# Kernel optimization log

Hardware: AMD Instinct MI355X
Metric: run time of the kernel (lower is better)

## Reference

```python
import jax, jax.numpy as jnp
import numpy as np

B, N, E = 8, 1000, 16000
HIST, PRED = 8, 12
IN_DIM = 14          # pm25(1) + met features(13)
HID_GAT, HEADS = 256, 8
GNN_OUT = 13
HID = 64             # GRU hidden (self.hid_dim = 64 in source)


def setup_inputs() -> dict:
    key = jax.random.key(0)
    ks = jax.random.split(key, 20)
    p = lambda k, shp, s=0.05: jax.random.normal(k, shp, dtype=jnp.float32) * s
    return {
        "pm25_hist": jax.random.normal(ks[0], (B, HIST, N, 1), dtype=jnp.float32),
        "feature": jax.random.normal(ks[1], (B, HIST + PRED, N, IN_DIM - 1), dtype=jnp.float32),
        "edge_index": jax.random.randint(ks[2], (2, E), 0, N),
        "gat1_W": p(ks[3], (IN_DIM, HEADS * HID_GAT)),
        "gat1_att_src": p(ks[4], (HEADS, HID_GAT)),
        "gat1_att_dst": p(ks[5], (HEADS, HID_GAT)),
        "gat1_b": p(ks[6], (HEADS * HID_GAT,)),
        "gat2_W": p(ks[7], (HEADS * HID_GAT, GNN_OUT)),
        "gat2_att_src": p(ks[8], (1, GNN_OUT)),
        "gat2_att_dst": p(ks[9], (1, GNN_OUT)),
        "gat2_b": p(ks[10], (GNN_OUT,)),
        "gru_W_ih": p(ks[11], (3 * HID, IN_DIM + GNN_OUT)),
        "gru_W_hh": p(ks[12], (3 * HID, HID)),
        "gru_b_ih": p(ks[13], (3 * HID,)),
        "gru_b_hh": p(ks[14], (3 * HID,)),
        "fc_out_W": p(ks[15], (HID, 1)),
        "fc_out_b": p(ks[16], (1,)),
    }


def _gat_conv(x, W, a_src, a_dst, b, src, dst, concat):
    # Single-graph GATConv (PyG semantics, eval mode: dropout disabled).
    # x: [N, F_in]; src/dst: [E'] (self-loops already appended)
    H, D = a_src.shape
    h = (x @ W).reshape(N, H, D)                       # [N, H, D]
    e = jax.nn.leaky_relu(
        (h * a_src).sum(-1)[src] + (h * a_dst).sum(-1)[dst], 0.2
    )                                                  # [E', H]
    # segment softmax over incoming edges of each dst node
    m = jax.ops.segment_max(e, dst, num_segments=N)
    ex = jnp.exp(e - m[dst])
    alpha = ex / jax.ops.segment_sum(ex, dst, num_segments=N)[dst]
    out = jax.ops.segment_sum(alpha[:, :, None] * h[src], dst, num_segments=N)  # [N, H, D]
    return (out.reshape(N, H * D) + b) if concat else (out.mean(1) + b)


def reference(pm25_hist, feature, edge_index,
              gat1_W, gat1_att_src, gat1_att_dst, gat1_b,
              gat2_W, gat2_att_src, gat2_att_dst, gat2_b,
              gru_W_ih, gru_W_hh, gru_b_ih, gru_b_hh,
              fc_out_W, fc_out_b):
    # add self-loops (PyG GATConv default)
    loop = jnp.arange(N)
    src = jnp.concatenate([edge_index[0], loop])
    dst = jnp.concatenate([edge_index[1], loop])

    def gnn(x):  # x: [N, IN_DIM] -> [N, GNN_OUT]
        h = jax.nn.elu(_gat_conv(x, gat1_W, gat1_att_src, gat1_att_dst, gat1_b, src, dst, True))
        return _gat_conv(h, gat2_W, gat2_att_src, gat2_att_dst, gat2_b, src, dst, False)

    gnn_b = jax.vmap(gnn)

    def gru(x, h):  # torch.nn.GRUCell math
        i_r, i_z, i_n = jnp.split(x @ gru_W_ih.T + gru_b_ih, 3, axis=-1)
        h_r, h_z, h_n = jnp.split(h @ gru_W_hh.T + gru_b_hh, 3, axis=-1)
        r = jax.nn.sigmoid(i_r + h_r)
        z = jax.nn.sigmoid(i_z + h_z)
        n = jnp.tanh(i_n + r * h_n)
        return (1.0 - z) * n + z * h

    feats = jnp.moveaxis(feature[:, HIST:HIST + PRED], 1, 0)  # [PRED, B, N, 13]

    def step(carry, f_t):
        hn, xn = carry
        x = jnp.concatenate([xn, f_t], axis=-1)               # [B, N, IN_DIM]
        g = gnn_b(x)                                          # [B, N, GNN_OUT]
        gx = jnp.concatenate([g, x], axis=-1).reshape(B * N, IN_DIM + GNN_OUT)
        hn = gru(gx, hn)                                      # [B*N, HID]
        xn = hn.reshape(B, N, HID) @ fc_out_W + fc_out_b      # [B, N, 1]
        return (hn, xn), xn

    h0 = jnp.zeros((B * N, HID), jnp.float32)
    xn0 = pm25_hist[:, -1]                                    # [B, N, 1]
    _, preds = jax.lax.scan(step, (h0, xn0), feats)
    return jnp.moveaxis(preds, 0, 1)                          # [B, PRED, N, 1]
```

## Files before the change

### kernel.cpp

```cpp
#include <hip/hip_runtime.h>
#include <hip/hip_bf16.h>
#include <math.h>

#define BB 8
#define NN 1000
#define EE 16000
#define ETOT 17000
#define TPRED 12
#define FEAT 13
#define INDIM 14
#define HEADS 8
#define HG 256
#define C1 2048
#define GO 13
#define HID 64

typedef unsigned int  uint32;
typedef unsigned short ushort16;
typedef uint32 uvec4 __attribute__((ext_vector_type(4)));
typedef __fp16 hf2 __attribute__((ext_vector_type(2)));

union U32H2 { uint32 u; hf2 h; };
__device__ __forceinline__ hf2 u2h(uint32 u){ U32H2 c; c.u=u; return c.h; }
__device__ __forceinline__ uint32 h2u(hf2 h){ U32H2 c; c.h=h; return c.u; }

#if __has_builtin(__builtin_amdgcn_fdot2)
__device__ __forceinline__ float FDOT2(hf2 a, hf2 b, float c){
    return __builtin_amdgcn_fdot2(a, b, c, false);
}
#else
__device__ __forceinline__ float FDOT2(hf2 a, hf2 b, float c){
    return c + (float)a.x*(float)b.x + (float)a.y*(float)b.y;
}
#endif

__device__ __forceinline__ float lrelu(float v){ return v > 0.f ? v : 0.2f*v; }

__device__ __forceinline__ ushort16 f2bf(float f){
    union { float f; uint32 u; } v; v.f = f;
    uint32 r = v.u + 0x7FFFu + ((v.u >> 16) & 1u);
    return (ushort16)(r >> 16);
}
__device__ __forceinline__ uint32 pack2(float lo, float hi){
    return (uint32)f2bf(lo) | ((uint32)f2bf(hi) << 16);
}
__device__ __forceinline__ void cvt2(uint32 u, float& lo, float& hi){
    union { uint32 u; float f; } a, b;
    a.u = u << 16; b.u = u & 0xFFFF0000u;
    lo = a.f; hi = b.f;
}


__global__ void k_att1pre(const float* W1, const float* asrc, const float* adst,
                          float* Wsrc, float* Wdst){
    int k = blockIdx.x >> 3, h = blockIdx.x & 7;
    int tid = threadIdx.x;
    float wv = W1[k*C1 + h*HG + tid];
    float ps = wv * asrc[h*HG + tid];
    float pd = wv * adst[h*HG + tid];
    #pragma unroll
    for (int m=1;m<64;m<<=1){ ps += __shfl_xor(ps,m); pd += __shfl_xor(pd,m); }
    __shared__ float rs[4], rd[4];
    int w = tid>>6;
    if ((tid&63)==0){ rs[w]=ps; rd[w]=pd; }
    __syncthreads();
    if (tid==0){
        Wsrc[k*8+h] = rs[0]+rs[1]+rs[2]+rs[3];
        Wdst[k*8+h] = rd[0]+rd[1]+rd[2]+rd[3];
    }
}

__global__ void k_packW1(const float* W1, uint32* w1pk){
    int i = blockIdx.x*blockDim.x + threadIdx.x;
    if (i < C1*8){
        int c = i >> 3, kk = i & 7;
        float lo = (kk < 7) ? W1[(2*kk)*C1 + c]   : 0.f;
        float hi = (kk < 7) ? W1[(2*kk+1)*C1 + c] : 0.f;
        w1pk[i] = h2u(__builtin_amdgcn_cvt_pkrtz(lo, hi));
    }
}

__global__ void k_att2pre(const float* W2, const float* a2s, const float* a2d,
                          uint32* w2pk){
    int m = blockIdx.x*blockDim.x + threadIdx.x;
    if (m < C1/2){
        int c0 = 2*m, c1 = 2*m+1;
        float colA[16], colB[16];
        float ssA=0.f, ddA=0.f, ssB=0.f, ddB=0.f;
        #pragma unroll
        for (int j=0;j<GO;j++){
            float wA = W2[c0*GO+j], wB = W2[c1*GO+j];
            colA[j]=wA; colB[j]=wB;
            ssA += wA*a2s[j]; ddA += wA*a2d[j];
            ssB += wB*a2s[j]; ddB += wB*a2d[j];
        }
        colA[13]=ssA; colA[14]=ddA; colA[15]=0.f;
        colB[13]=ssB; colB[14]=ddB; colB[15]=0.f;
        #pragma unroll
        for (int j=0;j<16;j++)
            w2pk[m*16+j] = h2u(__builtin_amdgcn_cvt_pkrtz(colA[j], colB[j]));
    }
}

__global__ void k_init(const float* pm25, const float* feat,
                       const float* Wsrc, const float* Wdst,
                       float* hn, float* xn, int* count,
                       float* ssrc, float* sdst, uint32* xpk){
    int i = blockIdx.x*blockDim.x + threadIdx.x;
    if (i < BB*NN*HID) hn[i] = 0.f;
    if (i < NN) count[i] = 0;
    if (i < BB*NN){
        int b = i/NN, n = i%NN;
        float x[INDIM];
        x[0] = pm25[(b*8 + 7)*NN + n];
        xn[i] = x[0];
        const float* fp = feat + ((size_t)(b*20 + 8)*NN + n)*FEAT;
        #pragma unroll
        for (int k=0;k<FEAT;k++) x[k+1] = fp[k];
        #pragma unroll
        for (int h=0;h<8;h++){
            float ss=0.f, dd=0.f;
            #pragma unroll
            for (int k=0;k<INDIM;k++){ ss += x[k]*Wsrc[k*8+h]; dd += x[k]*Wdst[k*8+h]; }
            ssrc[i*8+h] = ss; sdst[i*8+h] = dd;
        }
        #pragma unroll
        for (int p=0;p<7;p++) xpk[i*8+p] = pack2(x[2*p], x[2*p+1]);
        xpk[i*8+7] = 0u;
    }
}

__global__ void k_count(const int* ei, int* count){
    int e = blockIdx.x*blockDim.x + threadIdx.x;
    if (e < ETOT){
        int dst = (e<EE) ? ei[EE+e] : (e-EE);
        atomicAdd(&count[dst], 1);
    }
}

__global__ void k_scan(const int* count, int* offs, int* cursor){
    __shared__ int s[1024];
    int tid = threadIdx.x;
    int myc = (tid<NN) ? count[tid] : 0;
    s[tid] = myc;
    __syncthreads();
    for (int d=1; d<1024; d<<=1){
        int v = (tid>=d) ? s[tid-d] : 0;
        __syncthreads();
        s[tid] += v;
        __syncthreads();
    }
    if (tid<NN){
        int off = s[tid] - myc;
        offs[tid] = off; cursor[tid] = off;
    }
    if (tid==NN-1) offs[NN] = s[tid];
}

__global__ void k_fill(const int* ei, int* cursor, int* csr_src){
    int e = blockIdx.x*blockDim.x + threadIdx.x;
    if (e < ETOT){
        int src = (e<EE) ? ei[e]    : (e-EE);
        int dst = (e<EE) ? ei[EE+e] : (e-EE);
        int pos = atomicAdd(&cursor[dst], 1);
        csr_src[pos] = src;
    }
}


__global__ __launch_bounds__(64) void k_agg14(const uint32* xpk, const float* ssrc,
        const float* sdst, const int* offs, const int* csr, float* agg){
    int lane = threadIdx.x;
    int blk = blockIdx.x;
    int b = blk & 7, dstn = blk >> 3;
    int bn = b*NN + dstn;
    int base = offs[dstn], deg = offs[dstn+1]-base;
    int h = lane & 7, slot = lane >> 3;
    float sdd = sdst[bn*8 + h];
    float mloc = -1e30f;
    for (int i=slot;i<deg;i+=8){
        int s = csr[base+i];
        mloc = fmaxf(mloc, lrelu(ssrc[(b*NN+s)*8+h]+sdd));
    }
    mloc = fmaxf(mloc, __shfl_xor(mloc,8));
    mloc = fmaxf(mloc, __shfl_xor(mloc,16));
    mloc = fmaxf(mloc, __shfl_xor(mloc,32));
    float dloc = 0.f;
    for (int i=slot;i<deg;i+=8){
        int s = csr[base+i];
        dloc += __expf(lrelu(ssrc[(b*NN+s)*8+h]+sdd)-mloc);
    }
    dloc += __shfl_xor(dloc,8); dloc += __shfl_xor(dloc,16); dloc += __shfl_xor(dloc,32);
    float rden = 1.f/dloc;
    int kk = lane & 7, h2 = lane >> 3;
    float m2   = __shfl(mloc, h2);
    float r2   = __shfl(rden, h2);
    float sdd2 = __shfl(sdd,  h2);
    float a0=0.f, a1=0.f;
    for (int e=0;e<deg;e++){
        int s = csr[base+e];
        float sc = lrelu(ssrc[(b*NN+s)*8+h2] + sdd2);
        float al = __expf(sc - m2)*r2;
        float x0,x1; cvt2(xpk[(b*NN+s)*8+kk], x0, x1);
        a0 += al*x0; a1 += al*x1;
    }
    float2 st; st.x = a0; st.y = a1;
    *(float2*)(agg + (size_t)bn*128 + h2*16 + 2*kk) = st;
}

__global__ __launch_bounds__(256,1) void k_expand(const float* agg, const uint32* w1pk,
        const uint32* w2pk, const float* b1, float* h2o, float* s2s, float* s2d){
    int tid = threadIdx.x;
    int hh = tid >> 5;
    uint32 w1r[64];
    #pragma unroll
    for (int q=0;q<16;q++){
        uvec4 u = *(const uvec4*)(w1pk + tid*64 + 4*q);
        w1r[4*q]=u.x; w1r[4*q+1]=u.y; w1r[4*q+2]=u.z; w1r[4*q+3]=u.w;
    }
    uint32 w2r[64];
    #pragma unroll
    for (int q=0;q<16;q++){
        uvec4 u = *(const uvec4*)(w2pk + tid*64 + 4*q);
        w2r[4*q]=u.x; w2r[4*q+1]=u.y; w2r[4*q+2]=u.z; w2r[4*q+3]=u.w;
    }
    float b1r[8];
    #pragma unroll
    for (int j=0;j<8;j++) b1r[j] = b1[8*tid+j];
    __shared__ float sred[256*17];
    __shared__ float red2[64];
    for (int idx = blockIdx.x; idx < BB*NN; idx += gridDim.x){
        const float4* ap = (const float4*)(agg + (size_t)idx*128 + hh*16);
        float4 A0=ap[0], A1=ap[1], A2=ap[2], A3=ap[3];
        hf2 agh[7];
        agh[0]=__builtin_amdgcn_cvt_pkrtz(A0.x,A0.y);
        agh[1]=__builtin_amdgcn_cvt_pkrtz(A0.z,A0.w);
        agh[2]=__builtin_amdgcn_cvt_pkrtz(A1.x,A1.y);
        agh[3]=__builtin_amdgcn_cvt_pkrtz(A1.z,A1.w);
        agh[4]=__builtin_amdgcn_cvt_pkrtz(A2.x,A2.y);
        agh[5]=__builtin_amdgcn_cvt_pkrtz(A2.z,A2.w);
        agh[6]=__builtin_amdgcn_cvt_pkrtz(A3.x,A3.y);
        float v[8];
        #pragma unroll
        for (int j=0;j<8;j++){
            float s = b1r[j];
            #pragma unroll
            for (int kk=0;kk<7;kk++) s = FDOT2(agh[kk], u2h(w1r[j*8+kk]), s);
            v[j] = s > 0.f ? s : __expf(s) - 1.f;
        }
        hf2 vp[4];
        #pragma unroll
        for (int q=0;q<4;q++) vp[q] = __builtin_amdgcn_cvt_pkrtz(v[2*q], v[2*q+1]);
        #pragma unroll
        for (int j=0;j<16;j++){
            float s = 0.f;
            #pragma unroll
            for (int q=0;q<4;q++) s = FDOT2(vp[q], u2h(w2r[q*16+j]), s);
            sred[tid*17 + j] = s;
        }
        __syncthreads();
        int j = tid & 15, g = tid >> 4;
        float s = 0.f;
        #pragma unroll
        for (int i=0;i<16;i++) s += sred[(g + 16*i)*17 + j];
        s += __shfl_xor(s, 16);
        s += __shfl_xor(s, 32);
        int lane = tid & 63, w = tid >> 6;
        if (lane < 16) red2[w*16 + lane] = s;
        __syncthreads();
        if (tid < 15){
            float r = red2[tid] + red2[16+tid] + red2[32+tid] + red2[48+tid];
            if (tid < GO)      h2o[idx*GO + tid] = r;
            else if (tid==13)  s2s[idx] = r;
            else               s2d[idx] = r;
        }
        __syncthreads();
    }
}

__global__ __launch_bounds__(256) void k_tail(int t, int last,
        const float* feat, const int* offs, const int* csr,
        const float* h2, const float* s2src, const float* s2dst, const float* b2,
        const float* Wih, const float* Whh, const float* bih, const float* bhh,
        const float* fcw, const float* fcb, const float* Wsrc, const float* Wdst,
        float* hn, float* xn, float* out,
        float* ssrc, float* sdst, uint32* xpk){
    __shared__ float sWih[192*27];
    __shared__ float sWhh[192*65];
    __shared__ float sb[449];
    __shared__ float sWa[224];
    __shared__ float gxs[4][28];
    __shared__ float hs[4][64];
    int tid = threadIdx.x;
    for (int i=tid;i<192*27;i+=256) sWih[i] = Wih[i];
    for (int i=tid;i<192*64;i+=256) sWhh[(i>>6)*65 + (i&63)] = Whh[i];
    for (int i=tid;i<192;i+=256){ sb[i] = bih[i]; sb[192+i] = bhh[i]; }
    if (tid<64) sb[384+tid] = fcw[tid];
    if (tid==0) sb[448] = fcb[0];
    if (tid<112){ sWa[tid] = Wsrc[tid]; sWa[112+tid] = Wdst[tid]; }
    __syncthreads();
    int w = tid>>6, lane = tid&63;
    for (int i=0;i<4;i++){
        int bn = blockIdx.x*16 + i*4 + w;
        int b = bn/NN, n = bn%NN;
        int base = offs[n], deg = offs[n+1]-base;
        float sdd = s2dst[bn];
        float mloc = -1e30f;
        for (int e=lane;e<deg;e+=64){
            int s = csr[base+e];
            mloc = fmaxf(mloc, lrelu(s2src[b*NN+s] + sdd));
        }
        #pragma unroll
        for (int m=1;m<64;m<<=1) mloc = fmaxf(mloc, __shfl_xor(mloc,m));
        float dloc = 0.f;
        for (int e=lane;e<deg;e+=64){
            int s = csr[base+e];
            dloc += __expf(lrelu(s2src[b*NN+s] + sdd) - mloc);
        }
        #pragma unroll
        for (int m=1;m<64;m<<=1) dloc += __shfl_xor(dloc,m);
        float rdv = 1.f / dloc;
        float acc[GO];
        #pragma unroll
        for (int c=0;c<GO;c++) acc[c]=0.f;
        for (int e=lane;e<deg;e+=64){
            int s = csr[base+e];
            float al = __expf(lrelu(s2src[b*NN+s] + sdd) - mloc) * rdv;
            const float* hr = h2 + (size_t)(b*NN+s)*GO;
            #pragma unroll
            for (int c=0;c<GO;c++) acc[c] += al*hr[c];
        }
        #pragma unroll
        for (int c=0;c<GO;c++){
            #pragma unroll
            for (int m=1;m<64;m<<=1) acc[c] += __shfl_xor(acc[c],m);
        }
        if (lane==0){
            #pragma unroll
            for (int c=0;c<GO;c++) gxs[w][c] = acc[c] + b2[c];
            gxs[w][GO] = xn[bn];
        }
        if (lane>=14 && lane<27)
            gxs[w][lane] = feat[((size_t)(b*20 + 8 + t)*NN + n)*FEAT + (lane-14)];
        hs[w][lane] = hn[bn*HID + lane];
        __syncthreads();
        float ir = sb[lane], iz = sb[64+lane], inn = sb[128+lane];
        #pragma unroll
        for (int c=0;c<27;c++){
            float xv = gxs[w][c];
            ir  += sWih[lane*27        + c]*xv;
            iz  += sWih[(64+lane)*27   + c]*xv;
            inn += sWih[(128+lane)*27  + c]*xv;
        }
        float hr = sb[192+lane], hz = sb[256+lane], hnv = sb[320+lane];
        #pragma unroll
        for (int j=0;j<64;j++){
            float hv = hs[w][j];
            hr  += sWhh[lane*65        + j]*hv;
            hz  += sWhh[(64+lane)*65   + j]*hv;
            hnv += sWhh[(128+lane)*65  + j]*hv;
        }
        float r  = 1.f/(1.f+__expf(-(ir+hr)));
        float z  = 1.f/(1.f+__expf(-(iz+hz)));
        float nv = tanhf(inn + r*hnv);
        float hold = hs[w][lane];
        float hnew = (1.f - z)*nv + z*hold;
        hn[bn*HID+lane] = hnew;
        float xv = hnew * sb[384+lane];
        #pragma unroll
        for (int m=1;m<64;m<<=1) xv += __shfl_xor(xv,m);
        float res = xv + sb[448];
        if (lane==0){
            xn[bn] = res;
            out[(b*TPRED + t)*NN + n] = res;
        }
        if (!last){
            const float* fp = feat + ((size_t)(b*20 + 9 + t)*NN + n)*FEAT;
            if (lane < 16){
                int h = lane & 7;
                const float* Wa = (lane<8) ? sWa : sWa+112;
                float s = res * Wa[h];
                #pragma unroll
                for (int k=1;k<14;k++) s += fp[k-1]*Wa[k*8+h];
                if (lane<8) ssrc[bn*8+h] = s; else sdst[bn*8+h] = s;
            } else if (lane < 23){
                int p = lane - 16;
                float lo = (p==0) ? res : fp[2*p-1];
                float hi = fp[2*p];
                xpk[bn*8+p] = pack2(lo, hi);
            } else if (lane == 23){
                xpk[bn*8+7] = 0u;
            }
        }
        __syncthreads();
    }
}


extern "C" void kernel_launch(void* const* d_in, const int* in_sizes, int n_in,
                              void* d_out, int out_size, void* d_ws, size_t ws_size,
                              hipStream_t stream){
    const float* pm25 = (const float*)d_in[0];
    const float* feat = (const float*)d_in[1];
    const int*   ei   = (const int*)  d_in[2];
    const float* W1   = (const float*)d_in[3];
    const float* a1s  = (const float*)d_in[4];
    const float* a1d  = (const float*)d_in[5];
    const float* b1   = (const float*)d_in[6];
    const float* W2   = (const float*)d_in[7];
    const float* a2s  = (const float*)d_in[8];
    const float* a2d  = (const float*)d_in[9];
    const float* b2   = (const float*)d_in[10];
    const float* Wih  = (const float*)d_in[11];
    const float* Whh  = (const float*)d_in[12];
    const float* bih  = (const float*)d_in[13];
    const float* bhh  = (const float*)d_in[14];
    const float* fcw  = (const float*)d_in[15];
    const float* fcb  = (const float*)d_in[16];
    float* out = (float*)d_out;

    float* f = (float*)d_ws;
    size_t o = 0;
    float* ssrc1 = f+o; o += (size_t)BB*NN*8;
    float* sdst1 = f+o; o += (size_t)BB*NN*8;
    float* agg   = f+o; o += (size_t)BB*NN*128;
    float* h2    = f+o; o += (size_t)BB*NN*GO + 8;
    float* s2s   = f+o; o += (size_t)BB*NN;
    float* s2d   = f+o; o += (size_t)BB*NN;
    float* hn    = f+o; o += (size_t)BB*NN*HID;
    float* xn    = f+o; o += (size_t)BB*NN;
    float* Wsrc  = f+o; o += INDIM*8;
    float* Wdst  = f+o; o += INDIM*8;
    uint32* xpk  = (uint32*)(f+o); o += (size_t)BB*NN*8;
    uint32* w1pk = (uint32*)(f+o); o += (size_t)C1*8;
    uint32* w2pk = (uint32*)(f+o); o += (size_t)(C1/2)*16;
    int* ibase  = (int*)(f+o);
    int* count  = ibase;
    int* cursor = ibase + NN;
    int* offs   = ibase + 2*NN;
    int* csr    = ibase + 2*NN + NN + 1;

    k_att1pre<<<112, 256,0,stream>>>(W1, a1s, a1d, Wsrc, Wdst);
    k_packW1 <<<64,  256,0,stream>>>(W1, w1pk);
    k_att2pre<<<4,   256,0,stream>>>(W2, a2s, a2d, w2pk);
    k_init   <<<2000,256,0,stream>>>(pm25, feat, Wsrc, Wdst, hn, xn, count,
                                     ssrc1, sdst1, xpk);
    k_count  <<<67,  256,0,stream>>>(ei, count);
    k_scan   <<<1,  1024,0,stream>>>(count, offs, cursor);
    k_fill   <<<67,  256,0,stream>>>(ei, cursor, csr);

    for (int t=0; t<TPRED; t++){
        k_agg14  <<<8000, 64,0,stream>>>(xpk, ssrc1, sdst1, offs, csr, agg);
        k_expand <<<512, 256,0,stream>>>(agg, w1pk, w2pk, b1, h2, s2s, s2d);
        k_tail   <<<500, 256,0,stream>>>(t, (t==TPRED-1)?1:0, feat, offs, csr,
                                         h2, s2s, s2d, b2,
                                         Wih, Whh, bih, bhh, fcw, fcb, Wsrc, Wdst,
                                         hn, xn, out, ssrc1, sdst1, xpk);
    }
}
```

Baseline: 940.5 us.

## Use packed fp16 dot products and smaller LDS footprint in GRU tail kernel

The GRU tail kernel now stores W_ih, W_hh, the input vector and hidden state as packed fp16 pairs in shared memory and accumulates with fp16 dot2 instructions. This halves the per-block LDS footprint and the LDS reads in the matvec. Occupancy is raised via launch_bounds(256,4), and the grid doubles to 1000 blocks with 8 nodes each instead of 16. The cost is reduced GRU matvec precision and weight staging into LDS repeated across twice as many blocks.

```diff
diff --git a/kernel.cpp b/kernel.cpp
--- a/kernel.cpp
+++ b/kernel.cpp
@@ -48,6 +48,9 @@
     union { uint32 u; float f; } a, b;
     a.u = u << 16; b.u = u & 0xFFFF0000u;
     lo = a.f; hi = b.f;
+}
+__device__ __forceinline__ uint32 pkh(float lo, float hi){
+    hf2 h; h.x = (__fp16)lo; h.y = (__fp16)hi; return h2u(h);
 }
 
 
@@ -278,30 +281,39 @@
     }
 }
 
-__global__ __launch_bounds__(256) void k_tail(int t, int last,
+__global__ __launch_bounds__(256,4) void k_tail(int t, int last,
         const float* feat, const int* offs, const int* csr,
         const float* h2, const float* s2src, const float* s2dst, const float* b2,
         const float* Wih, const float* Whh, const float* bih, const float* bhh,
         const float* fcw, const float* fcb, const float* Wsrc, const float* Wdst,
         float* hn, float* xn, float* out,
         float* ssrc, float* sdst, uint32* xpk){
-    __shared__ float sWih[192*27];
-    __shared__ float sWhh[192*65];
-    __shared__ float sb[449];
-    __shared__ float sWa[224];
-    __shared__ float gxs[4][28];
-    __shared__ float hs[4][64];
+    __shared__ uint32 sWihP[192*14];
+    __shared__ uint32 sWhhP[192*33];
+    __shared__ float  sb[449];
+    __shared__ float  sWa[224];
+    __shared__ float  gxs[4][28];
+    __shared__ uint32 gxsP[4][14];
+    __shared__ uint32 hsP[4][32];
     int tid = threadIdx.x;
-    for (int i=tid;i<192*27;i+=256) sWih[i] = Wih[i];
-    for (int i=tid;i<192*64;i+=256) sWhh[(i>>6)*65 + (i&63)] = Whh[i];
+    for (int i=tid;i<192*14;i+=256){
+        int r = i/14, c2 = i - r*14;
+        float lo = Wih[r*27 + 2*c2];
+        float hi = (2*c2+1 < 27) ? Wih[r*27 + 2*c2 + 1] : 0.f;
+        sWihP[i] = pkh(lo, hi);
+    }
+    for (int i=tid;i<192*32;i+=256){
+        int r = i>>5, j2 = i&31;
+        sWhhP[r*33 + j2] = pkh(Whh[r*64 + 2*j2], Whh[r*64 + 2*j2 + 1]);
+    }
     for (int i=tid;i<192;i+=256){ sb[i] = bih[i]; sb[192+i] = bhh[i]; }
     if (tid<64) sb[384+tid] = fcw[tid];
     if (tid==0) sb[448] = fcb[0];
     if (tid<112){ sWa[tid] = Wsrc[tid]; sWa[112+tid] = Wdst[tid]; }
     __syncthreads();
     int w = tid>>6, lane = tid&63;
-    for (int i=0;i<4;i++){
-        int bn = blockIdx.x*16 + i*4 + w;
+    for (int i=0;i<2;i++){
+        int bn = blockIdx.x*8 + i*4 + w;
         int b = bn/NN, n = bn%NN;
         int base = offs[n], deg = offs[n+1]-base;
         float sdd = s2dst[bn];
@@ -326,9 +338,9 @@
         for (int e=lane;e<deg;e+=64){
             int s = csr[base+e];
             float al = __expf(lrelu(s2src[b*NN+s] + sdd) - mloc) * rdv;
-            const float* hr = h2 + (size_t)(b*NN+s)*GO;
-            #pragma unroll
-            for (int c=0;c<GO;c++) acc[c] += al*hr[c];
+            const float* hr2 = h2 + (size_t)(b*NN+s)*GO;
+            #pragma unroll
+            for (int c=0;c<GO;c++) acc[c] += al*hr2[c];
         }
         #pragma unroll
         for (int c=0;c<GO;c++){
@@ -339,31 +351,35 @@
             #pragma unroll
             for (int c=0;c<GO;c++) gxs[w][c] = acc[c] + b2[c];
             gxs[w][GO] = xn[bn];
+            gxs[w][27] = 0.f;
         }
         if (lane>=14 && lane<27)
             gxs[w][lane] = feat[((size_t)(b*20 + 8 + t)*NN + n)*FEAT + (lane-14)];
-        hs[w][lane] = hn[bn*HID + lane];
+        if (lane<32)
+            hsP[w][lane] = pkh(hn[bn*HID + 2*lane], hn[bn*HID + 2*lane + 1]);
+        float hold = hn[bn*HID + lane];
+        __syncthreads();
+        if (lane<14) gxsP[w][lane] = pkh(gxs[w][2*lane], gxs[w][2*lane+1]);
         __syncthreads();
         float ir = sb[lane], iz = sb[64+lane], inn = sb[128+lane];
         #pragma unroll
-        for (int c=0;c<27;c++){
-            float xv = gxs[w][c];
-            ir  += sWih[lane*27        + c]*xv;
-            iz  += sWih[(64+lane)*27   + c]*xv;
-            inn += sWih[(128+lane)*27  + c]*xv;
+        for (int c2=0;c2<14;c2++){
+            hf2 g2 = u2h(gxsP[w][c2]);
+            ir  = FDOT2(g2, u2h(sWihP[lane*14        + c2]), ir);
+            iz  = FDOT2(g2, u2h(sWihP[(64+lane)*14   + c2]), iz);
+            inn = FDOT2(g2, u2h(sWihP[(128+lane)*14  + c2]), inn);
         }
         float hr = sb[192+lane], hz = sb[256+lane], hnv = sb[320+lane];
         #pragma unroll
-        for (int j=0;j<64;j++){
-            float hv = hs[w][j];
-            hr  += sWhh[lane*65        + j]*hv;
-            hz  += sWhh[(64+lane)*65   + j]*hv;
-            hnv += sWhh[(128+lane)*65  + j]*hv;
+        for (int j2=0;j2<32;j2++){
+            hf2 h2v = u2h(hsP[w][j2]);
+            hr  = FDOT2(h2v, u2h(sWhhP[lane*33        + j2]), hr);
+            hz  = FDOT2(h2v, u2h(sWhhP[(64+lane)*33   + j2]), hz);
+            hnv = FDOT2(h2v, u2h(sWhhP[(128+lane)*33  + j2]), hnv);
         }
         float r  = 1.f/(1.f+__expf(-(ir+hr)));
         float z  = 1.f/(1.f+__expf(-(iz+hz)));
         float nv = tanhf(inn + r*hnv);
-        float hold = hs[w][lane];
         float hnew = (1.f - z)*nv + z*hold;
         hn[bn*HID+lane] = hnew;
         float xv = hnew * sb[384+lane];
@@ -452,7 +468,7 @@
     for (int t=0; t<TPRED; t++){
         k_agg14  <<<8000, 64,0,stream>>>(xpk, ssrc1, sdst1, offs, csr, agg);
         k_expand <<<512, 256,0,stream>>>(agg, w1pk, w2pk, b1, h2, s2s, s2d);
-        k_tail   <<<500, 256,0,stream>>>(t, (t==TPRED-1)?1:0, feat, offs, csr,
+        k_tail   <<<1000,256,0,stream>>>(t, (t==TPRED-1)?1:0, feat, offs, csr,
                                          h2, s2s, s2d, b2,
                                          Wih, Whh, bih, bhh, fcw, fcb, Wsrc, Wdst,
                                          hn, xn, out, ssrc1, sdst1, xpk);
```

After: 1.008 ms. 7.2% more time.
